# Kernel tuning notes

Hardware: AMD Instinct MI355X
Metric: run time of the kernel (lower is better)

The kernel has to match this reference:

```python
import jax, jax.numpy as jnp
import numpy as np

BITS = 4
GROUPSIZE = 128
IN_FEATURES = 4096
OUT_FEATURES = 11008
N_GROUPS = IN_FEATURES // GROUPSIZE  # 32
MASK = (1 << BITS) - 1  # 15


def setup_inputs() -> dict:
    key = jax.random.key(0)
    ks = jax.random.split(key, 5)
    x = jax.random.normal(ks[0], (2, 2048, IN_FEATURES), dtype=jnp.float32)
    qweight = jax.random.randint(ks[1], (IN_FEATURES // 8, OUT_FEATURES), 0, 2**31 - 1, dtype=jnp.int32)
    qzeros = jax.random.randint(ks[2], (N_GROUPS, OUT_FEATURES // 8), 0, 2**31 - 1, dtype=jnp.int32)
    scales = jax.random.uniform(ks[3], (N_GROUPS, OUT_FEATURES), dtype=jnp.float16)
    bias = jax.random.normal(ks[4], (OUT_FEATURES,), dtype=jnp.float32)
    return {"x": x, "qweight": qweight, "qzeros": qzeros, "scales": scales, "bias": bias}


def _dequant(qweight, qzeros, scales):
    # wf = [0, 4, 8, ..., 28]: bit offsets of the 8 int4 nibbles in each int32
    wf = jnp.arange(0, 32, BITS, dtype=jnp.int32)
    # unpack weights: [IN//8, OUT] -> [IN//8, 8, OUT] -> [N_GROUPS, GROUPSIZE, OUT]
    w = (qweight[:, None, :] >> wf[None, :, None]) & MASK
    w = w.reshape(N_GROUPS, GROUPSIZE, OUT_FEATURES).astype(jnp.float32)
    # unpack zeros: [NG, OUT//8] -> [NG, OUT//8, 8] -> [NG, 1, OUT]
    z = (qzeros[:, :, None] >> wf[None, None, :]) & MASK
    z = z.reshape(N_GROUPS, 1, OUT_FEATURES).astype(jnp.float32)
    s = scales.astype(jnp.float32)[:, None, :]  # [NG, 1, OUT]
    # scales * w - scales * z, per group; fused elementwise
    return (s * (w - z)).reshape(IN_FEATURES, OUT_FEATURES)


def reference(x, qweight, qzeros, scales, bias):
    W = _dequant(qweight, qzeros, scales)  # [IN, OUT] fp32
    out = jnp.matmul(x.astype(jnp.float32), W) + bias
    return out
```

## Files before the change

### kernel.cpp

```cpp
#include <hip/hip_runtime.h>
#include <hip/hip_fp16.h>

#define K_DIM 4096
#define N_DIM 11008
#define NZ8   1376
#define BM    256
#define BN    256
#define NT_N  43
#define NKT   64
#define ATB   32768

typedef _Float16 f16x8 __attribute__((ext_vector_type(8)));
typedef float    f32x4 __attribute__((ext_vector_type(4)));

#define SB()    __builtin_amdgcn_sched_barrier(0)
#define BAR()   __builtin_amdgcn_s_barrier()
#define VMW(N)  do { asm volatile("s_waitcnt vmcnt(" #N ")" ::: "memory"); SB(); } while (0)
#define LGKM0() do { asm volatile("s_waitcnt lgkmcnt(0)" ::: "memory"); SB(); } while (0)

__device__ __forceinline__ f16x8 dq8(unsigned q, __half2 scp, __half2 nzp)
{
    const unsigned mu = 0xE400E400u;
    const __half2 m1024 = *(const __half2*)&mu;
    union { __half2 h2[4]; f16x8 v; } p;
#pragma unroll
    for (int d = 0; d < 4; ++d) {
        unsigned t = ((q >> (4 * d)) & 0x000F000Fu) | 0x64006400u;
        p.h2[d] = __hfma2(__hadd2(*(const __half2*)&t, m1024), scp, nzp);
    }
    return p.v;
}

__device__ __forceinline__ void mk_scp(unsigned su, unsigned zu, int ngl,
                                       __half2& scp, __half2& nzp)
{
    const float sc = __uint_as_float(su);
    const float zf = (float)((zu >> ((ngl & 7) * 4)) & 15u);
    const __half sh = __float2half_rn(sc), nh = __float2half_rn(-sc * zf);
    scp = __half2(sh, sh); nzp = __half2(nh, nh);
}

__global__ __launch_bounds__(256)
void r13_xcvt(const float* __restrict__ x, __half* __restrict__ xh, int nchunks)
{
    int c = blockIdx.x * 256 + threadIdx.x;
    const int stride = gridDim.x * 256;
    for (; c < nchunks; c += stride) {
        const int row = c & 255;
        const int sl  = (c >> 8) & 3;
        const int kh  = (c >> 10) & 1;
        const int tl  = c >> 11;
        const int mt  = tl >> 6;
        const int kt  = tl & 63;
        const size_t gm = (size_t)mt * 256 + row;
        const int kb = kt * 64 + kh * 32 + sl * 8;
        const float4 f0 = *(const float4*)(x + gm * K_DIM + kb);
        const float4 f1 = *(const float4*)(x + gm * K_DIM + kb + 4);
        union { __half2 h2[4]; int4 v; } p;
        p.h2[0] = __floats2half2_rn(f0.x, f1.x);
        p.h2[1] = __floats2half2_rn(f0.y, f1.y);
        p.h2[2] = __floats2half2_rn(f0.z, f1.z);
        p.h2[3] = __floats2half2_rn(f0.w, f1.w);
        ((int4*)xh)[c] = p.v;
    }
}

#define ISSUE_Q(D0, D1, T, H) do { \
    const int* _a0 = qwp + (size_t)((T) * 8 + 4 * (H)) * N_DIM; \
    const int* _a1 = qwp + (size_t)((T) * 8 + 4 * (H) + 2) * N_DIM; \
    asm volatile("global_load_dword %0, %2, off\n\t" \
                 "global_load_dword %1, %3, off" \
                 : "=&v"(D0), "=&v"(D1) : "v"(_a0), "v"(_a1) : "memory"); \
} while (0)

#define ISSUE_S(DS, DZ, G) do { \
    const float* _sa = scales + (size_t)(G) * N_DIM + ngl; \
    const int*   _za = qzeros + (size_t)(G) * NZ8 + (ngl >> 3); \
    asm volatile("global_load_dword %0, %2, off\n\t" \
                 "global_load_dword %1, %3, off" \
                 : "=&v"(DS), "=&v"(DZ) : "v"(_sa), "v"(_za) : "memory"); \
} while (0)

#define ISSUE_A(BUFP, T, H) do { \
    const char* _s = agp + (size_t)(T) * ATB + (H) * 16384; \
    __builtin_amdgcn_global_load_lds((const unsigned int*)_s, \
        (unsigned int*)((BUFP) + (H) * 16384 + tid * 16), 16, 0, 0); \
    __builtin_amdgcn_global_load_lds((const unsigned int*)(_s + 8192), \
        (unsigned int*)((BUFP) + (H) * 16384 + tid * 16 + 8192), 16, 0, 0); \
} while (0)

#define FRAGS(ARp, BRp, KH) do { \
    _Pragma("unroll") for (int m = 0; m < 8; ++m) \
        af[m] = *(const f16x8*)((ARp) + (KH) * 16384 + aOff + m * 256); \
    _Pragma("unroll") for (int n = 0; n < 4; ++n) \
        bf[n] = *(const f16x8*)((BRp) + (KH) * 16384 + bOff + n * 256); \
} while (0)

#define MFMA32() do { \
    __builtin_amdgcn_s_setprio(1); \
    _Pragma("unroll") for (int m = 0; m < 8; ++m) \
        _Pragma("unroll") for (int n = 0; n < 4; ++n) \
            acc[m][n] = __builtin_amdgcn_mfma_f32_16x16x32_f16(af[m], bf[n], acc[m][n], 0, 0, 0); \
    __builtin_amdgcn_s_setprio(0); \
    SB(); \
} while (0)

#define DQ2(BWp, H, Q0, Q1) do { \
    *(f16x8*)((BWp) + (H) * 16384 + bq * 4096 + bnn * 16)       = dq8(Q0, scp, nzp); \
    *(f16x8*)((BWp) + (H) * 16384 + (bq + 2) * 4096 + bnn * 16) = dq8(Q1, scp, nzp); \
} while (0)

__global__ __launch_bounds__(512, 2)
void r13_gemm(const __half* __restrict__ xh,
              const int*   __restrict__ qweight,
              const int*   __restrict__ qzeros,
              const float* __restrict__ scales,
              const float* __restrict__ bias,
              float* __restrict__ out)
{
    __shared__ __align__(16) unsigned char A0s[ATB], A1s[ATB];
    __shared__ __align__(16) unsigned char B0s[ATB], B1s[ATB];

    const int tid  = threadIdx.x;
    const int lane = tid & 63;
    const int wid  = tid >> 6;
    const int wr   = (wid >> 2) * 128;
    const int wc   = (wid & 3) * 64;

    int bid = blockIdx.x;
    const int cpx = gridDim.x >> 3;
    bid = (bid & 7) * cpx + (bid >> 3);
    const int bm0 = (bid / NT_N) * BM;
    const int bn0 = (bid % NT_N) * BN;

    const int bnn = tid & 255;
    const int bq  = tid >> 8;
    const int ngl = bn0 + bnn;
    const int* qwp = qweight + (size_t)bq * N_DIM + ngl;
    const char* agp = (const char*)xh + ((size_t)(bm0 >> 8) * NKT) * ATB + tid * 16;

    const int frow = lane & 15, kb8 = lane >> 4;
    const int aOff = kb8 * 4096 + (wr + frow) * 16;
    const int bOff = kb8 * 4096 + (wc + frow) * 16;

    unsigned char *aR = A0s, *aW = A1s, *bR = B0s, *bW = B1s;

    f32x4 acc[8][4];
#pragma unroll
    for (int m = 0; m < 8; ++m)
#pragma unroll
        for (int n = 0; n < 4; ++n)
            acc[m][n] = (f32x4){0.f, 0.f, 0.f, 0.f};
    f16x8 af[8], bf[4];
    __half2 scp, nzp;
    unsigned qc0, qc1, qc2, qc3, qn0, qn1, qn2, qn3;
    unsigned sSc2, sZq2;

    unsigned sSc0 = __float_as_uint(scales[ngl]);
    unsigned sZq0 = (unsigned)qzeros[ngl >> 3];
    unsigned sSc1 = __float_as_uint(scales[(size_t)N_DIM + ngl]);
    unsigned sZq1 = (unsigned)qzeros[NZ8 + (ngl >> 3)];
    asm volatile("" : "+v"(sSc0), "+v"(sZq0), "+v"(sSc1), "+v"(sZq1));
    VMW(0);
    unsigned q00, q01, q02, q03;
    ISSUE_Q(q00, q01, 0, 0);
    ISSUE_Q(q02, q03, 0, 1);
    ISSUE_A(aR, 0, 0); SB();
    ISSUE_Q(qc0, qc1, 1, 0);
    ISSUE_A(aR, 0, 1);
    ISSUE_Q(qc2, qc3, 1, 1);
    ISSUE_A(aW, 1, 0); SB();
    VMW(10);
    mk_scp(sSc0, sZq0, ngl, scp, nzp);
    DQ2(bR, 0, q00, q01);
    DQ2(bR, 1, q02, q03);
    LGKM0(); VMW(8);
    BAR();

    for (int u = 0; u < 31; ++u) {
        const int t0 = 2 * u;
        mk_scp(sSc0, sZq0, ngl, scp, nzp);
        FRAGS(aR, bR, 0); SB();
        ISSUE_Q(qn0, qn1, t0 + 2, 0);
        ISSUE_A(aW, t0 + 1, 1); SB();
        VMW(10);
        DQ2(bW, 0, qc0, qc1);
        LGKM0(); VMW(8);
        BAR();
        MFMA32();
        FRAGS(aR, bR, 1); SB();
        ISSUE_Q(qn2, qn3, t0 + 2, 1);
        ISSUE_A(aR, t0 + 2, 0);
        { const int gS = (u + 2 <= 31) ? (u + 2) : 31; ISSUE_S(sSc2, sZq2, gS); }
        SB();
        VMW(12);
        DQ2(bW, 1, qc2, qc3);
        LGKM0(); VMW(10);
        BAR();
        MFMA32();
        { unsigned char* tp = aR; aR = aW; aW = tp; }
        { unsigned char* tp = bR; bR = bW; bW = tp; }
        qc0 = qn0; qc1 = qn1; qc2 = qn2; qc3 = qn3;
        mk_scp(sSc1, sZq1, ngl, scp, nzp);
        FRAGS(aR, bR, 0); SB();
        ISSUE_Q(qn0, qn1, t0 + 3, 0);
        ISSUE_A(aW, t0 + 2, 1); SB();
        VMW(12);
        DQ2(bW, 0, qc0, qc1);
        LGKM0(); VMW(10);
        BAR();
        MFMA32();
        FRAGS(aR, bR, 1); SB();
        ISSUE_Q(qn2, qn3, t0 + 3, 1);
        ISSUE_A(aR, t0 + 3, 0); SB();
        VMW(12);
        DQ2(bW, 1, qc2, qc3);
        LGKM0(); VMW(10);
        BAR();
        MFMA32();
        { unsigned char* tp = aR; aR = aW; aW = tp; }
        { unsigned char* tp = bR; bR = bW; bW = tp; }
        qc0 = qn0; qc1 = qn1; qc2 = qn2; qc3 = qn3;
        sSc0 = sSc1; sZq0 = sZq1; sSc1 = sSc2; sZq1 = sZq2;
    }

    mk_scp(sSc0, sZq0, ngl, scp, nzp);
    FRAGS(aR, bR, 0); SB();
    ISSUE_A(aW, 63, 1); SB();
    VMW(8);
    DQ2(bW, 0, qc0, qc1);
    LGKM0(); VMW(6);
    BAR();
    MFMA32();
    FRAGS(aR, bR, 1); SB();
    VMW(4);
    DQ2(bW, 1, qc2, qc3);
    LGKM0(); VMW(2);
    BAR();
    MFMA32();
    { unsigned char* tp = aR; aR = aW; aW = tp; }
    { unsigned char* tp = bR; bR = bW; bW = tp; }
    FRAGS(aR, bR, 0);
    MFMA32();
    VMW(0);
    BAR();
    FRAGS(aR, bR, 1);
    MFMA32();

    const int crow0 = (lane >> 4) << 2, ccol = lane & 15;
#pragma unroll
    for (int n = 0; n < 4; ++n) {
        const int col = bn0 + wc + n * 16 + ccol;
        const float bv = bias[col];
#pragma unroll
        for (int m = 0; m < 8; ++m) {
            const int row = bm0 + wr + m * 16 + crow0;
#pragma unroll
            for (int j = 0; j < 4; ++j)
                out[(size_t)(row + j) * N_DIM + col] = acc[m][n][j] + bv;
        }
    }
}

typedef __bf16 bf16x8 __attribute__((ext_vector_type(8)));

__global__ __launch_bounds__(256, 2)
void r13_fb(const float* __restrict__ x,
            const int*   __restrict__ qweight,
            const int*   __restrict__ qzeros,
            const float* __restrict__ scales,
            const float* __restrict__ bias,
            float* __restrict__ out)
{
    __shared__ __align__(16) unsigned char Asm[128 * 64 * 2];
    __shared__ __align__(16) unsigned char Bsm[128 * 64 * 2];
    const int tid = threadIdx.x, lane = tid & 63, wv = tid >> 6;
    const int wr = (wv >> 1) * 64, wc = (wv & 1) * 64;
    int bid = blockIdx.x;
    const int cpx = gridDim.x >> 3;
    bid = (bid & 7) * cpx + (bid >> 3);
    const int bm0 = (bid / 86) * 128, bn0 = (bid % 86) * 128;
    const int ar = tid >> 4, ac4 = tid & 15;
    const float* xp = x + (size_t)(bm0 + ar) * K_DIM + ac4 * 4;
    unsigned char* aw = Asm + ar * 128 + ((ac4 * 8) ^ ((ar & 7) << 4));
    const int bnn = tid & 127, bk8q = tid >> 7, ngl = bn0 + bnn;
    const int* qwp = qweight + (size_t)bk8q * N_DIM + ngl;
    unsigned char* bw = Bsm + bnn * 128;
    const int bsw = bnn & 7;
    const int frow = lane & 15, kb8 = lane >> 4, fsw = frow & 7;
    f32x4 acc[4][4];
#pragma unroll
    for (int m = 0; m < 4; ++m)
#pragma unroll
        for (int n = 0; n < 4; ++n) acc[m][n] = (f32x4){0.f, 0.f, 0.f, 0.f};
    float sc = 0.f, nsz = 0.f;
    for (int kt = 0; kt < K_DIM / 64; ++kt) {
        const int k0 = kt * 64;
        if ((k0 & 127) == 0) {
            const int g = k0 >> 7;
            sc = scales[(size_t)g * N_DIM + ngl];
            const unsigned zq = (unsigned)qzeros[(size_t)g * NZ8 + (ngl >> 3)];
            nsz = -sc * (float)((zq >> ((ngl & 7) * 4)) & 15u);
        }
#pragma unroll
        for (int i = 0; i < 8; ++i) {
            const float4 v = *(const float4*)(xp + (size_t)i * 16 * K_DIM + k0);
            union { __bf16 h[4]; unsigned long long u; } p;
            p.h[0] = (__bf16)v.x; p.h[1] = (__bf16)v.y;
            p.h[2] = (__bf16)v.z; p.h[3] = (__bf16)v.w;
            *(unsigned long long*)(aw + i * 16 * 128) = p.u;
        }
#pragma unroll
        for (int i = 0; i < 4; ++i) {
            const int k8 = 2 * i + bk8q;
            const unsigned q = (unsigned)qwp[(size_t)(kt * 8 + 2 * i) * N_DIM];
            union { __bf16 h[8]; bf16x8 v8; } p;
#pragma unroll
            for (int j = 0; j < 8; ++j)
                p.h[j] = (__bf16)__builtin_fmaf(sc, (float)((q >> (4 * j)) & 15u), nsz);
            *(bf16x8*)(bw + ((k8 ^ bsw) << 4)) = p.v8;
        }
        __syncthreads();
#pragma unroll
        for (int kh = 0; kh < 2; ++kh) {
            const int ksl = (kh << 2) + kb8;
            bf16x8 a2[4], b2[4];
#pragma unroll
            for (int m = 0; m < 4; ++m)
                a2[m] = *(const bf16x8*)(Asm + (wr + m * 16 + frow) * 128 + ((ksl ^ fsw) << 4));
#pragma unroll
            for (int n = 0; n < 4; ++n)
                b2[n] = *(const bf16x8*)(Bsm + (wc + n * 16 + frow) * 128 + ((ksl ^ fsw) << 4));
#pragma unroll
            for (int m = 0; m < 4; ++m)
#pragma unroll
                for (int n = 0; n < 4; ++n)
                    acc[m][n] = __builtin_amdgcn_mfma_f32_16x16x32_bf16(a2[m], b2[n], acc[m][n], 0, 0, 0);
        }
        __syncthreads();
    }
    const int crow0 = (lane >> 4) << 2, ccol = lane & 15;
#pragma unroll
    for (int n = 0; n < 4; ++n) {
        const int col = bn0 + wc + n * 16 + ccol;
        const float bv = bias[col];
#pragma unroll
        for (int m = 0; m < 4; ++m) {
            const int row = bm0 + wr + m * 16 + crow0;
#pragma unroll
            for (int j = 0; j < 4; ++j)
                out[(size_t)(row + j) * N_DIM + col] = acc[m][n][j] + bv;
        }
    }
}

extern "C" void kernel_launch(void* const* d_in, const int* in_sizes, int n_in,
                              void* d_out, int out_size, void* d_ws, size_t ws_size,
                              hipStream_t stream)
{
    const float* x   = (const float*)d_in[0];
    const int*   qw  = (const int*)d_in[1];
    const int*   qz  = (const int*)d_in[2];
    const float* scl = (const float*)d_in[3];
    const float* bs  = (const float*)d_in[4];
    float* out = (float*)d_out;

    const int M = in_sizes[0] / K_DIM;
    const size_t xh_bytes = (size_t)M * K_DIM * 2;

    if (ws_size >= xh_bytes) {
        __half* xh = (__half*)d_ws;
        const int nchunks = M * K_DIM / 8;
        hipLaunchKernelGGL(r13_xcvt, dim3(2048), dim3(256), 0, stream, x, xh, nchunks);
        dim3 grid((M / BM) * NT_N);
        hipLaunchKernelGGL(r13_gemm, grid, dim3(512), 0, stream,
                           xh, qw, qz, scl, bs, out);
    } else {
        dim3 grid((M / 128) * 86);
        hipLaunchKernelGGL(r13_fb, grid, dim3(256), 0, stream,
                           x, qw, qz, scl, bs, out);
    }
}
```

Measured before the change: 387.4 us.

## Dequantize int4 weights directly into MFMA B fragments, dropping LDS staging for B

Each wave now loads the packed qweight words it needs for its own B fragments straight into registers and dequantizes them in place, instead of cooperatively dequantizing into a double-buffered LDS B tile and reading fragments back. This removes the B LDS buffers (halving shared memory), the LDS writes and reads for B, and half of the barriers per k-step. In exchange, qweight, scales and zeros are loaded redundantly across the two wave rows, so global and L2 traffic for them doubles. The extra prefetch registers may also hurt occupancy or cause spills.

```diff
diff --git a/kernel.cpp b/kernel.cpp
--- a/kernel.cpp
+++ b/kernel.cpp
@@ -31,17 +31,8 @@
     return p.v;
 }
 
-__device__ __forceinline__ void mk_scp(unsigned su, unsigned zu, int ngl,
-                                       __half2& scp, __half2& nzp)
-{
-    const float sc = __uint_as_float(su);
-    const float zf = (float)((zu >> ((ngl & 7) * 4)) & 15u);
-    const __half sh = __float2half_rn(sc), nh = __float2half_rn(-sc * zf);
-    scp = __half2(sh, sh); nzp = __half2(nh, nh);
-}
-
 __global__ __launch_bounds__(256)
-void r13_xcvt(const float* __restrict__ x, __half* __restrict__ xh, int nchunks)
+void r15_xcvt(const float* __restrict__ x, __half* __restrict__ xh, int nchunks)
 {
     int c = blockIdx.x * 256 + threadIdx.x;
     const int stride = gridDim.x * 256;
@@ -65,35 +56,53 @@
     }
 }
 
-#define ISSUE_Q(D0, D1, T, H) do { \
-    const int* _a0 = qwp + (size_t)((T) * 8 + 4 * (H)) * N_DIM; \
-    const int* _a1 = qwp + (size_t)((T) * 8 + 4 * (H) + 2) * N_DIM; \
-    asm volatile("global_load_dword %0, %2, off\n\t" \
-                 "global_load_dword %1, %3, off" \
-                 : "=&v"(D0), "=&v"(D1) : "v"(_a0), "v"(_a1) : "memory"); \
-} while (0)
-
-#define ISSUE_S(DS, DZ, G) do { \
-    const float* _sa = scales + (size_t)(G) * N_DIM + ngl; \
-    const int*   _za = qzeros + (size_t)(G) * NZ8 + (ngl >> 3); \
-    asm volatile("global_load_dword %0, %2, off\n\t" \
-                 "global_load_dword %1, %3, off" \
-                 : "=&v"(DS), "=&v"(DZ) : "v"(_sa), "v"(_za) : "memory"); \
-} while (0)
-
-#define ISSUE_A(BUFP, T, H) do { \
-    const char* _s = agp + (size_t)(T) * ATB + (H) * 16384; \
-    __builtin_amdgcn_global_load_lds((const unsigned int*)_s, \
-        (unsigned int*)((BUFP) + (H) * 16384 + tid * 16), 16, 0, 0); \
-    __builtin_amdgcn_global_load_lds((const unsigned int*)(_s + 8192), \
-        (unsigned int*)((BUFP) + (H) * 16384 + tid * 16 + 8192), 16, 0, 0); \
-} while (0)
-
-#define FRAGS(ARp, BRp, KH) do { \
+#define ISSUE_Q8(D0,D1,D2,D3,D4,D5,D6,D7) do { \
+    asm volatile( \
+        "global_load_dword %0, %8, off\n\t" \
+        "global_load_dword %1, %8, off offset:64\n\t" \
+        "global_load_dword %2, %8, off offset:128\n\t" \
+        "global_load_dword %3, %8, off offset:192\n\t" \
+        "global_load_dword %4, %9, off\n\t" \
+        "global_load_dword %5, %9, off offset:64\n\t" \
+        "global_load_dword %6, %9, off offset:128\n\t" \
+        "global_load_dword %7, %9, off offset:192" \
+        : "=&v"(D0), "=&v"(D1), "=&v"(D2), "=&v"(D3), \
+          "=&v"(D4), "=&v"(D5), "=&v"(D6), "=&v"(D7) \
+        : "v"(qp0), "v"(qp1) : "memory"); \
+    qp0 += 8 * N_DIM; qp1 += 8 * N_DIM; \
+} while (0)
+
+#define ISSUE_SZ() do { \
+    asm volatile( \
+        "global_load_dword %0, %8, off\n\t" \
+        "global_load_dword %1, %8, off offset:64\n\t" \
+        "global_load_dword %2, %8, off offset:128\n\t" \
+        "global_load_dword %3, %8, off offset:192\n\t" \
+        "global_load_dword %4, %9, off\n\t" \
+        "global_load_dword %5, %9, off offset:8\n\t" \
+        "global_load_dword %6, %9, off offset:16\n\t" \
+        "global_load_dword %7, %9, off offset:24" \
+        : "=&v"(sS0), "=&v"(sS1), "=&v"(sS2), "=&v"(sS3), \
+          "=&v"(sZ0), "=&v"(sZ1), "=&v"(sZ2), "=&v"(sZ3) \
+        : "v"(sp), "v"(zp) : "memory"); \
+    sp += N_DIM; zp += NZ8; \
+} while (0)
+
+#define ISSUE_A(BUFP, T) do { \
+    const char* _s = agp + (size_t)(T) * ATB; \
+    _Pragma("unroll") for (int j = 0; j < 4; ++j) \
+        __builtin_amdgcn_global_load_lds((const unsigned int*)(_s + j * 8192), \
+            (unsigned int*)((BUFP) + j * 8192 + tid * 16), 16, 0, 0); \
+} while (0)
+
+#define FRAGS(ARp, KH) do { \
     _Pragma("unroll") for (int m = 0; m < 8; ++m) \
         af[m] = *(const f16x8*)((ARp) + (KH) * 16384 + aOff + m * 256); \
-    _Pragma("unroll") for (int n = 0; n < 4; ++n) \
-        bf[n] = *(const f16x8*)((BRp) + (KH) * 16384 + bOff + n * 256); \
+} while (0)
+
+#define DQ4(Q0,Q1,Q2,Q3) do { \
+    bf[0] = dq8(Q0, scp0, nzp0); bf[1] = dq8(Q1, scp1, nzp1); \
+    bf[2] = dq8(Q2, scp2, nzp2); bf[3] = dq8(Q3, scp3, nzp3); \
 } while (0)
 
 #define MFMA32() do { \
@@ -105,13 +114,23 @@
     SB(); \
 } while (0)
 
-#define DQ2(BWp, H, Q0, Q1) do { \
-    *(f16x8*)((BWp) + (H) * 16384 + bq * 4096 + bnn * 16)       = dq8(Q0, scp, nzp); \
-    *(f16x8*)((BWp) + (H) * 16384 + (bq + 2) * 4096 + bnn * 16) = dq8(Q1, scp, nzp); \
+#define CVT_S() do { \
+    const float _s0 = __uint_as_float(sS0), _s1 = __uint_as_float(sS1); \
+    const float _s2 = __uint_as_float(sS2), _s3 = __uint_as_float(sS3); \
+    const __half _h0 = __float2half_rn(_s0), _h1 = __float2half_rn(_s1); \
+    const __half _h2 = __float2half_rn(_s2), _h3 = __float2half_rn(_s3); \
+    scp0 = __half2(_h0, _h0); scp1 = __half2(_h1, _h1); \
+    scp2 = __half2(_h2, _h2); scp3 = __half2(_h3, _h3); \
+    const __half _n0 = __float2half_rn(-_s0 * (float)((sZ0 >> sh4) & 15u)); \
+    const __half _n1 = __float2half_rn(-_s1 * (float)((sZ1 >> sh4) & 15u)); \
+    const __half _n2 = __float2half_rn(-_s2 * (float)((sZ2 >> sh4) & 15u)); \
+    const __half _n3 = __float2half_rn(-_s3 * (float)((sZ3 >> sh4) & 15u)); \
+    nzp0 = __half2(_n0, _n0); nzp1 = __half2(_n1, _n1); \
+    nzp2 = __half2(_n2, _n2); nzp3 = __half2(_n3, _n3); \
 } while (0)
 
 __global__ __launch_bounds__(512, 2)
-void r13_gemm(const __half* __restrict__ xh,
+void r15_gemm(const __half* __restrict__ xh,
               const int*   __restrict__ qweight,
               const int*   __restrict__ qzeros,
               const float* __restrict__ scales,
@@ -119,7 +138,6 @@
               float* __restrict__ out)
 {
     __shared__ __align__(16) unsigned char A0s[ATB], A1s[ATB];
-    __shared__ __align__(16) unsigned char B0s[ATB], B1s[ATB];
 
     const int tid  = threadIdx.x;
     const int lane = tid & 63;
@@ -133,17 +151,19 @@
     const int bm0 = (bid / NT_N) * BM;
     const int bn0 = (bid % NT_N) * BN;
 
-    const int bnn = tid & 255;
-    const int bq  = tid >> 8;
-    const int ngl = bn0 + bnn;
-    const int* qwp = qweight + (size_t)bq * N_DIM + ngl;
+    const int frow = lane & 15, kb8 = lane >> 4;
+    const int ngl2 = bn0 + wc + frow;
+    const int sh4  = (ngl2 & 7) * 4;
+    const int aOff = kb8 * 4096 + (wr + frow) * 16;
+
     const char* agp = (const char*)xh + ((size_t)(bm0 >> 8) * NKT) * ATB + tid * 16;
 
-    const int frow = lane & 15, kb8 = lane >> 4;
-    const int aOff = kb8 * 4096 + (wr + frow) * 16;
-    const int bOff = kb8 * 4096 + (wc + frow) * 16;
-
-    unsigned char *aR = A0s, *aW = A1s, *bR = B0s, *bW = B1s;
+    const int*   qp0 = qweight + (size_t)kb8 * N_DIM + ngl2;
+    const int*   qp1 = qweight + (size_t)(kb8 + 4) * N_DIM + ngl2;
+    const float* sp  = scales + (size_t)N_DIM + ngl2;
+    const int*   zp  = qzeros + (size_t)NZ8 + (ngl2 >> 3);
+
+    unsigned char *aR = A0s, *aW = A1s;
 
     f32x4 acc[8][4];
 #pragma unroll
@@ -152,100 +172,59 @@
         for (int n = 0; n < 4; ++n)
             acc[m][n] = (f32x4){0.f, 0.f, 0.f, 0.f};
     f16x8 af[8], bf[4];
-    __half2 scp, nzp;
-    unsigned qc0, qc1, qc2, qc3, qn0, qn1, qn2, qn3;
-    unsigned sSc2, sZq2;
-
-    unsigned sSc0 = __float_as_uint(scales[ngl]);
-    unsigned sZq0 = (unsigned)qzeros[ngl >> 3];
-    unsigned sSc1 = __float_as_uint(scales[(size_t)N_DIM + ngl]);
-    unsigned sZq1 = (unsigned)qzeros[NZ8 + (ngl >> 3)];
-    asm volatile("" : "+v"(sSc0), "+v"(sZq0), "+v"(sSc1), "+v"(sZq1));
+    __half2 scp0, scp1, scp2, scp3, nzp0, nzp1, nzp2, nzp3;
+    unsigned qa0, qa1, qa2, qa3, qa4, qa5, qa6, qa7;
+    unsigned qb0, qb1, qb2, qb3, qb4, qb5, qb6, qb7;
+    unsigned sS0, sS1, sS2, sS3, sZ0, sZ1, sZ2, sZ3;
+
+    sS0 = __float_as_uint(scales[ngl2]);
+    sS1 = __float_as_uint(scales[ngl2 + 16]);
+    sS2 = __float_as_uint(scales[ngl2 + 32]);
+    sS3 = __float_as_uint(scales[ngl2 + 48]);
+    sZ0 = (unsigned)qzeros[(ngl2 >> 3) + 0];
+    sZ1 = (unsigned)qzeros[(ngl2 >> 3) + 2];
+    sZ2 = (unsigned)qzeros[(ngl2 >> 3) + 4];
+    sZ3 = (unsigned)qzeros[(ngl2 >> 3) + 6];
+    asm volatile("" : "+v"(sS0), "+v"(sS1), "+v"(sS2), "+v"(sS3),
+                      "+v"(sZ0), "+v"(sZ1), "+v"(sZ2), "+v"(sZ3));
     VMW(0);
-    unsigned q00, q01, q02, q03;
-    ISSUE_Q(q00, q01, 0, 0);
-    ISSUE_Q(q02, q03, 0, 1);
-    ISSUE_A(aR, 0, 0); SB();
-    ISSUE_Q(qc0, qc1, 1, 0);
-    ISSUE_A(aR, 0, 1);
-    ISSUE_Q(qc2, qc3, 1, 1);
-    ISSUE_A(aW, 1, 0); SB();
-    VMW(10);
-    mk_scp(sSc0, sZq0, ngl, scp, nzp);
-    DQ2(bR, 0, q00, q01);
-    DQ2(bR, 1, q02, q03);
-    LGKM0(); VMW(8);
+    ISSUE_Q8(qa0, qa1, qa2, qa3, qa4, qa5, qa6, qa7);
+    ISSUE_A(aR, 0);
+    ISSUE_Q8(qb0, qb1, qb2, qb3, qb4, qb5, qb6, qb7);
+    ISSUE_A(aW, 1);
+    VMW(12);
     BAR();
 
     for (int u = 0; u < 31; ++u) {
         const int t0 = 2 * u;
-        mk_scp(sSc0, sZq0, ngl, scp, nzp);
-        FRAGS(aR, bR, 0); SB();
-        ISSUE_Q(qn0, qn1, t0 + 2, 0);
-        ISSUE_A(aW, t0 + 1, 1); SB();
-        VMW(10);
-        DQ2(bW, 0, qc0, qc1);
-        LGKM0(); VMW(8);
-        BAR();
-        MFMA32();
-        FRAGS(aR, bR, 1); SB();
-        ISSUE_Q(qn2, qn3, t0 + 2, 1);
-        ISSUE_A(aR, t0 + 2, 0);
-        { const int gS = (u + 2 <= 31) ? (u + 2) : 31; ISSUE_S(sSc2, sZq2, gS); }
-        SB();
-        VMW(12);
-        DQ2(bW, 1, qc2, qc3);
-        LGKM0(); VMW(10);
-        BAR();
-        MFMA32();
+        CVT_S();
+        FRAGS(aR, 0); DQ4(qa0, qa1, qa2, qa3); LGKM0(); MFMA32();
+        FRAGS(aR, 1); DQ4(qa4, qa5, qa6, qa7);
+        ISSUE_Q8(qa0, qa1, qa2, qa3, qa4, qa5, qa6, qa7);
+        ISSUE_SZ();
+        LGKM0(); MFMA32();
+        VMW(16);
+        BAR(); SB();
         { unsigned char* tp = aR; aR = aW; aW = tp; }
-        { unsigned char* tp = bR; bR = bW; bW = tp; }
-        qc0 = qn0; qc1 = qn1; qc2 = qn2; qc3 = qn3;
-        mk_scp(sSc1, sZq1, ngl, scp, nzp);
-        FRAGS(aR, bR, 0); SB();
-        ISSUE_Q(qn0, qn1, t0 + 3, 0);
-        ISSUE_A(aW, t0 + 2, 1); SB();
-        VMW(12);
-        DQ2(bW, 0, qc0, qc1);
-        LGKM0(); VMW(10);
-        BAR();
-        MFMA32();
-        FRAGS(aR, bR, 1); SB();
-        ISSUE_Q(qn2, qn3, t0 + 3, 1);
-        ISSUE_A(aR, t0 + 3, 0); SB();
-        VMW(12);
-        DQ2(bW, 1, qc2, qc3);
-        LGKM0(); VMW(10);
-        BAR();
-        MFMA32();
+        ISSUE_A(aW, t0 + 2);
+        FRAGS(aR, 0); DQ4(qb0, qb1, qb2, qb3); LGKM0(); MFMA32();
+        FRAGS(aR, 1); DQ4(qb4, qb5, qb6, qb7);
+        ISSUE_Q8(qb0, qb1, qb2, qb3, qb4, qb5, qb6, qb7);
+        LGKM0(); MFMA32();
+        VMW(8);
+        BAR(); SB();
         { unsigned char* tp = aR; aR = aW; aW = tp; }
-        { unsigned char* tp = bR; bR = bW; bW = tp; }
-        qc0 = qn0; qc1 = qn1; qc2 = qn2; qc3 = qn3;
-        sSc0 = sSc1; sZq0 = sZq1; sSc1 = sSc2; sZq1 = sZq2;
-    }
-
-    mk_scp(sSc0, sZq0, ngl, scp, nzp);
-    FRAGS(aR, bR, 0); SB();
-    ISSUE_A(aW, 63, 1); SB();
-    VMW(8);
-    DQ2(bW, 0, qc0, qc1);
-    LGKM0(); VMW(6);
-    BAR();
-    MFMA32();
-    FRAGS(aR, bR, 1); SB();
-    VMW(4);
-    DQ2(bW, 1, qc2, qc3);
-    LGKM0(); VMW(2);
-    BAR();
-    MFMA32();
+        ISSUE_A(aW, t0 + 3);
+    }
+
+    CVT_S();
+    FRAGS(aR, 0); DQ4(qa0, qa1, qa2, qa3); LGKM0(); MFMA32();
+    FRAGS(aR, 1); DQ4(qa4, qa5, qa6, qa7); LGKM0(); MFMA32();
+    VMW(0);
+    BAR(); SB();
     { unsigned char* tp = aR; aR = aW; aW = tp; }
-    { unsigned char* tp = bR; bR = bW; bW = tp; }
-    FRAGS(aR, bR, 0);
-    MFMA32();
-    VMW(0);
-    BAR();
-    FRAGS(aR, bR, 1);
-    MFMA32();
+    FRAGS(aR, 0); DQ4(qb0, qb1, qb2, qb3); LGKM0(); MFMA32();
+    FRAGS(aR, 1); DQ4(qb4, qb5, qb6, qb7); LGKM0(); MFMA32();
 
     const int crow0 = (lane >> 4) << 2, ccol = lane & 15;
 #pragma unroll
@@ -265,7 +244,7 @@
 typedef __bf16 bf16x8 __attribute__((ext_vector_type(8)));
 
 __global__ __launch_bounds__(256, 2)
-void r13_fb(const float* __restrict__ x,
+void r15_fb(const float* __restrict__ x,
             const int*   __restrict__ qweight,
             const int*   __restrict__ qzeros,
             const float* __restrict__ scales,
@@ -371,13 +350,13 @@
     if (ws_size >= xh_bytes) {
         __half* xh = (__half*)d_ws;
         const int nchunks = M * K_DIM / 8;
-        hipLaunchKernelGGL(r13_xcvt, dim3(2048), dim3(256), 0, stream, x, xh, nchunks);
+        hipLaunchKernelGGL(r15_xcvt, dim3(2048), dim3(256), 0, stream, x, xh, nchunks);
         dim3 grid((M / BM) * NT_N);
-        hipLaunchKernelGGL(r13_gemm, grid, dim3(512), 0, stream,
+        hipLaunchKernelGGL(r15_gemm, grid, dim3(512), 0, stream,
                            xh, qw, qz, scl, bs, out);
     } else {
         dim3 grid((M / 128) * 86);
-        hipLaunchKernelGGL(r13_fb, grid, dim3(256), 0, stream,
+        hipLaunchKernelGGL(r15_fb, grid, dim3(256), 0, stream,
                            x, qw, qz, scl, bs, out);
     }
 }
```

New measurement: 386.2 us. About the same (-0.3%).
